# Performance work log

Measured on AMD Instinct MI355X. Metric: run time of the kernel, lower is better.

Reference implementation:

```python
import jax, jax.numpy as jnp
import numpy as np

N, E, D, H, ED = 50000, 600000, 128, 2, 5
C = D // H  # per-head channels = 64


def _lin(k, fan_in, fan_out):
    return jax.random.normal(k, (fan_out, fan_in), jnp.float32) / np.sqrt(fan_in)


def setup_inputs() -> dict:
    key = jax.random.key(0)
    ks = jax.random.split(key, 12)
    return {
        "x": jax.random.normal(ks[0], (N, D), jnp.float32),
        "edge_index": jax.random.randint(ks[1], (2, E), 0, N, dtype=jnp.int32),
        "edge_attr": jax.random.normal(ks[2], (E, ED), jnp.float32),
        "Wq": _lin(ks[3], D, D), "bq": jnp.zeros((D,), jnp.float32),
        "Wk": _lin(ks[4], D, D), "bk": jnp.zeros((D,), jnp.float32),
        "Wv": _lin(ks[5], D, D), "bv": jnp.zeros((D,), jnp.float32),
        "We": _lin(ks[6], ED, D),                       # lin_edge, bias=False in PyG
        "Wskip": _lin(ks[7], D, D), "bskip": jnp.zeros((D,), jnp.float32),
        "Wbeta": _lin(ks[8], 3 * D, 1),                 # lin_beta, bias=False
        "Wproj": _lin(ks[9], D, D), "bproj": jnp.zeros((D,), jnp.float32),
    }


def reference(x, edge_index, edge_attr, Wq, bq, Wk, bk, Wv, bv, We,
              Wskip, bskip, Wbeta, Wproj, bproj):
    src, dst = edge_index[0], edge_index[1]
    # node projections -> [N, H, C]
    q = (x @ Wq.T + bq).reshape(N, H, C)
    k = (x @ Wk.T + bk).reshape(N, H, C)
    v = (x @ Wv.T + bv).reshape(N, H, C)
    e = (edge_attr @ We.T).reshape(E, H, C)
    # gather per-edge, fold in edge features
    kj = k[src] + e                                   # [E, H, C]
    vj = v[src] + e                                   # [E, H, C]
    alpha = (q[dst] * kj).sum(-1) / np.sqrt(C)        # [E, H]
    # segment softmax over edges grouped by dst node
    amax = jax.ops.segment_max(alpha, dst, num_segments=N)   # [N, H]
    ex = jnp.exp(alpha - amax[dst])
    denom = jax.ops.segment_sum(ex, dst, num_segments=N)     # [N, H]
    w = ex / denom[dst]                               # [E, H]
    # scatter-aggregate weighted values, concat heads
    out = jax.ops.segment_sum(vj * w[:, :, None], dst, num_segments=N).reshape(N, D)
    # beta-gated skip connection
    x_r = x @ Wskip.T + bskip
    beta = jax.nn.sigmoid(jnp.concatenate([out, x_r, out - x_r], axis=-1) @ Wbeta.T)  # [N,1]
    out = beta * x_r + (1.0 - beta) * out
    # outer projection (dropout is identity in eval)
    return out @ Wproj.T + bproj
```

## Files before the change

### kernel.cpp

```cpp
#include <hip/hip_runtime.h>
#include <stdint.h>
#include <math.h>

#define D 128
#define EDIM 5
#define QSCALE 0.1803368801111204f

typedef __attribute__((ext_vector_type(8))) short bf16x8;
typedef __attribute__((ext_vector_type(4))) float f32x4;
typedef _Float16 h16x2 __attribute__((ext_vector_type(2)));

__device__ __forceinline__ float fexp2(float x) {
  return __builtin_amdgcn_exp2f(x);
}

__device__ __forceinline__ ushort f2b(float f) {
  union { float f; uint u; } v; v.f = f;
  uint u = v.u;
  return (ushort)((u + 0x7fff + ((u >> 16) & 1)) >> 16);
}
__device__ __forceinline__ float blo(uint u) {
  union { uint u; float f; } v; v.u = u << 16; return v.f;
}
__device__ __forceinline__ float bhi(uint u) {
  union { uint u; float f; } v; v.u = u & 0xffff0000u; return v.f;
}
__device__ __forceinline__ ushort f2h(float f) {
  union { _Float16 h; ushort u; } v; v.h = (_Float16)f;
  return v.u;
}
__device__ __forceinline__ h16x2 u2h(uint u) {
  union { uint u; h16x2 h; } v; v.u = u; return v.h;
}

#if __has_builtin(__builtin_amdgcn_fdot2)
#define FDOT2(a, b, c) __builtin_amdgcn_fdot2((a), (b), (c), false)
#else
#define FDOT2(a, b, c) ((c) + (float)(a)[0] * (float)(b)[0] + (float)(a)[1] * (float)(b)[1])
#endif


__global__ void hist_kernel(const int* __restrict__ ei, int* __restrict__ deg, int E) {
  int e = blockIdx.x * blockDim.x + threadIdx.x;
  if (e < E) atomicAdd(&deg[ei[(size_t)E + e]], 1);
}

__global__ __launch_bounds__(256) void scan_p1(const int* __restrict__ deg,
                                               int* __restrict__ off,
                                               int* __restrict__ blockSum, int n4) {
  __shared__ int waveTot[4];
  int idx = blockIdx.x * 256 + threadIdx.x;
  int4 v = make_int4(0, 0, 0, 0);
  if (idx < n4) v = ((const int4*)deg)[idx];
  int c0 = v.x, c1 = c0 + v.y, c2 = c1 + v.z, c3 = c2 + v.w;
  int tot = c3;
  int lane = threadIdx.x & 63, w = threadIdx.x >> 6;
  int incl = tot;
#pragma unroll
  for (int ofs = 1; ofs < 64; ofs <<= 1) {
    int t = __shfl_up(incl, ofs, 64);
    if (lane >= ofs) incl += t;
  }
  if (lane == 63) waveTot[w] = incl;
  __syncthreads();
  int wbase = 0;
  for (int i = 0; i < w; ++i) wbase += waveTot[i];
  int excl = wbase + incl - tot;
  if (idx < n4) {
    int4 o;
    o.x = excl; o.y = excl + c0; o.z = excl + c1; o.w = excl + c2;
    ((int4*)off)[idx] = o;
  }
  if (threadIdx.x == 255) blockSum[blockIdx.x] = wbase + incl;
}

__global__ void scan_p2(const int* __restrict__ blockSum, int* __restrict__ blockBase,
                        int* __restrict__ off_last, int nb) {
  int lane = threadIdx.x;
  int v = (lane < nb) ? blockSum[lane] : 0;
  int incl = v;
#pragma unroll
  for (int ofs = 1; ofs < 64; ofs <<= 1) {
    int t = __shfl_up(incl, ofs, 64);
    if (lane >= ofs) incl += t;
  }
  if (lane < nb) blockBase[lane] = incl - v;
  if (lane == 63) *off_last = incl;
}

__global__ __launch_bounds__(256) void scan_p3(int* __restrict__ off,
                                               const int* __restrict__ blockBase,
                                               int* __restrict__ cursor, int n4) {
  int idx = blockIdx.x * 256 + threadIdx.x;
  if (idx >= n4) return;
  int b = blockBase[blockIdx.x];
  int4 v = ((int4*)off)[idx];
  v.x += b; v.y += b; v.z += b; v.w += b;
  ((int4*)off)[idx] = v;
  ((int4*)cursor)[idx] = make_int4(0, 0, 0, 0);
}

__global__ void scatter_kernel(const int* __restrict__ ei, const float* __restrict__ ea,
                               const int* __restrict__ off, int* __restrict__ cursor,
                               uint4* __restrict__ easrt, int E) {
  int e = blockIdx.x * blockDim.x + threadIdx.x;
  if (e >= E) return;
  int dst = ei[(size_t)E + e];
  int pos = off[dst] + atomicAdd(&cursor[dst], 1);
  const float* p = ea + (size_t)e * EDIM;
  uint e0 = f2b(p[0]), e1 = f2b(p[1]), e2 = f2b(p[2]), e3 = f2b(p[3]), e4 = f2b(p[4]);
  easrt[pos] = make_uint4(e0 | (e1 << 16), e2 | (e3 << 16), e4, (uint)ei[e]);
}

__global__ void cvt_w_kernel(const float* __restrict__ Wq, const float* __restrict__ Wk,
                             const float* __restrict__ Wv, const float* __restrict__ Wr,
                             const float* __restrict__ bq, const float* __restrict__ bk,
                             const float* __restrict__ bv, const float* __restrict__ br,
                             const float* __restrict__ We, const float* __restrict__ Wp,
                             ushort* __restrict__ Wcat, float* __restrict__ bcat,
                             ushort* __restrict__ Wpb, int* __restrict__ deg, int N) {
  int i = blockIdx.x * blockDim.x + threadIdx.x;
  if (i < N) deg[i] = 0;
  if (i < 512 * D) {
    int r = i >> 7;
    float v;
    if (r < 128)      v = Wq[i] * QSCALE;
    else if (r < 256) v = Wk[i - 128 * D];
    else if (r < 384) v = Wv[i - 256 * D];
    else              v = Wr[i - 384 * D];
    Wcat[i] = f2b(v);
  } else if (i < 512 * D + 128 * D) {
    int ie = i - 512 * D;
    int r = ie >> 7, c = ie & 127;
    int h = r >> 3, j = r & 7;
    float v = 0.f;
    if (h < 2 && j < 5) {
      for (int d = 0; d < 64; ++d) {
        int dd = h * 64 + d;
        v += We[(size_t)dd * EDIM + j] * QSCALE * Wq[(size_t)dd * D + c];
      }
    }
    Wcat[(size_t)(512 + r) * D + c] = f2b(v);
  }
  if (i < D * D) Wpb[i] = f2b(Wp[i]);
  if (i < 512) {
    float v = (i < 128) ? bq[i] * QSCALE
            : (i < 256) ? bk[i - 128]
            : (i < 384) ? bv[i - 256] : br[i - 384];
    bcat[i] = v;
  } else if (i < 640) {
    int t = i - 512;
    int h = t >> 3, j = t & 7;
    float v = 0.f;
    if (h < 2 && j < 5) {
      for (int d = 0; d < 64; ++d) {
        int dd = h * 64 + d;
        v += bq[dd] * QSCALE * We[(size_t)dd * EDIM + j];
      }
    }
    bcat[i] = v;
  }
}

__global__ __launch_bounds__(256) void proj_gemm_kernel(
    const float* __restrict__ x, const ushort* __restrict__ Wcat,
    const float* __restrict__ bcat,
    ushort* __restrict__ q, ushort* __restrict__ kv, ushort* __restrict__ xr,
    float* __restrict__ qwe, int M)
{
  __shared__ __attribute__((aligned(16))) ushort As[64][128];
  __shared__ __attribute__((aligned(16))) ushort Bs[128][128];
  const int tid = threadIdx.x;
  const int rowBase = blockIdx.x * 64;

#pragma unroll
  for (int it = 0; it < 4; ++it) {
    int i = it * 256 + tid;
    int r = i >> 4, c = i & 15;
    int gr = rowBase + r;
    float4 a0 = make_float4(0.f, 0.f, 0.f, 0.f), a1 = a0;
    if (gr < M) {
      a0 = *(const float4*)(x + (size_t)gr * D + c * 8);
      a1 = *(const float4*)(x + (size_t)gr * D + c * 8 + 4);
    }
    uint4 w;
    w.x = (uint)f2b(a0.x) | ((uint)f2b(a0.y) << 16);
    w.y = (uint)f2b(a0.z) | ((uint)f2b(a0.w) << 16);
    w.z = (uint)f2b(a1.x) | ((uint)f2b(a1.y) << 16);
    w.w = (uint)f2b(a1.z) | ((uint)f2b(a1.w) << 16);
    *(uint4*)(&As[r][(c ^ (r & 7)) * 8]) = w;
  }

  const int lane = tid & 63;
  const int wave = tid >> 6;
  const int wm = (wave >> 1) * 32;
  const int wn = (wave & 1) * 64;
  const int lrow = lane & 15;
  const int kgrp = lane >> 4;
  const int orow = (lane >> 4) * 4;
  const int ocol = lane & 15;

  for (int cb = 0; cb < 5; ++cb) {
#pragma unroll
    for (int it = 0; it < 8; ++it) {
      int i = it * 256 + tid;
      int r = i >> 4, c = i & 15;
      if (cb == 4 && r >= 16) continue;
      uint4 bv4 = *(const uint4*)(Wcat + (size_t)(cb * 128 + r) * D + c * 8);
      *(uint4*)(&Bs[r][(c ^ (r & 7)) * 8]) = bv4;
    }
    __syncthreads();

    f32x4 acc[2][4] = {};
#pragma unroll
    for (int ks = 0; ks < 4; ++ks) {
      int chunk = ks * 4 + kgrp;
      bf16x8 a[2], b[4];
#pragma unroll
      for (int m = 0; m < 2; ++m) {
        int r = wm + m * 16 + lrow;
        a[m] = *(const bf16x8*)&As[r][(chunk ^ (r & 7)) * 8];
      }
#pragma unroll
      for (int n = 0; n < 4; ++n) {
        int r = wn + n * 16 + lrow;
        b[n] = *(const bf16x8*)&Bs[r][(chunk ^ (r & 7)) * 8];
      }
#pragma unroll
      for (int m = 0; m < 2; ++m)
#pragma unroll
        for (int n = 0; n < 4; ++n) {
          if (cb == 4 && (wn + n * 16) >= 16) continue;
          acc[m][n] = __builtin_amdgcn_mfma_f32_16x16x32_bf16(a[m], b[n], acc[m][n], 0, 0, 0);
        }
    }

#pragma unroll
    for (int m = 0; m < 2; ++m) {
#pragma unroll
      for (int n = 0; n < 4; ++n) {
        if (cb == 4 && (wn + n * 16) >= 16) continue;
        int col = cb * 128 + wn + n * 16 + ocol;
        float bi = bcat[col];
        int sel = col >> 7, c = col & 127;
#pragma unroll
        for (int ii = 0; ii < 4; ++ii) {
          int gr = rowBase + wm + m * 16 + orow + ii;
          if (gr >= M) continue;
          float v = acc[m][n][ii] + bi;
          if (sel == 0)      q[(size_t)gr * D + c] = f2h(v);
          else if (sel == 1) kv[(size_t)gr * 2 * D + c] = f2h(v);
          else if (sel == 2) kv[(size_t)gr * 2 * D + D + c] = f2h(v);
          else if (sel == 3) xr[(size_t)gr * D + c] = f2b(v);
          else if (c < 16)   qwe[(size_t)gr * 16 + c] = v;
        }
      }
    }
    __syncthreads();
  }
}

__global__ __launch_bounds__(256) void out_gemm_kernel(
    const ushort* __restrict__ g, const ushort* __restrict__ Wpb,
    const float* __restrict__ bp, float* __restrict__ out, int M)
{
  __shared__ __attribute__((aligned(16))) ushort As[64][128];
  __shared__ __attribute__((aligned(16))) ushort Bs[128][128];
  const int tid = threadIdx.x;
  const int rowBase = blockIdx.x * 64;

#pragma unroll
  for (int it = 0; it < 4; ++it) {
    int i = it * 256 + tid;
    int r = i >> 4, c = i & 15;
    int gr = rowBase + r;
    uint4 av = make_uint4(0, 0, 0, 0);
    if (gr < M) av = *(const uint4*)(g + (size_t)gr * D + c * 8);
    *(uint4*)(&As[r][(c ^ (r & 7)) * 8]) = av;
  }
#pragma unroll
  for (int it = 0; it < 8; ++it) {
    int i = it * 256 + tid;
    int r = i >> 4, c = i & 15;
    uint4 bv4 = *(const uint4*)(Wpb + (size_t)r * D + c * 8);
    *(uint4*)(&Bs[r][(c ^ (r & 7)) * 8]) = bv4;
  }
  __syncthreads();

  const int lane = tid & 63;
  const int wave = tid >> 6;
  const int wm = (wave >> 1) * 32;
  const int wn = (wave & 1) * 64;
  const int lrow = lane & 15;
  const int kgrp = lane >> 4;

  f32x4 acc[2][4] = {};
#pragma unroll
  for (int ks = 0; ks < 4; ++ks) {
    int chunk = ks * 4 + kgrp;
    bf16x8 a[2], b[4];
#pragma unroll
    for (int m = 0; m < 2; ++m) {
      int r = wm + m * 16 + lrow;
      a[m] = *(const bf16x8*)&As[r][(chunk ^ (r & 7)) * 8];
    }
#pragma unroll
    for (int n = 0; n < 4; ++n) {
      int r = wn + n * 16 + lrow;
      b[n] = *(const bf16x8*)&Bs[r][(chunk ^ (r & 7)) * 8];
    }
#pragma unroll
    for (int m = 0; m < 2; ++m)
#pragma unroll
      for (int n = 0; n < 4; ++n)
        acc[m][n] = __builtin_amdgcn_mfma_f32_16x16x32_bf16(a[m], b[n], acc[m][n], 0, 0, 0);
  }

  const int orow = (lane >> 4) * 4;
  const int ocol = lane & 15;
#pragma unroll
  for (int m = 0; m < 2; ++m) {
#pragma unroll
    for (int n = 0; n < 4; ++n) {
      int col = wn + n * 16 + ocol;
      float bi = bp[col];
#pragma unroll
      for (int ii = 0; ii < 4; ++ii) {
        int gr = rowBase + wm + m * 16 + orow + ii;
        if (gr >= M) continue;
        out[(size_t)gr * D + col] = acc[m][n][ii] + bi;
      }
    }
  }
}

__global__ __launch_bounds__(256) void node_attn_kernel(
    const ushort* __restrict__ q, const ushort* __restrict__ kv,
    const ushort* __restrict__ xr, ushort* __restrict__ g,
    const float* __restrict__ qwe, const uint4* __restrict__ easrt,
    const float* __restrict__ We, const float* __restrict__ Wb,
    const int* __restrict__ off, int N)
{
  const int wid = threadIdx.x >> 6;
  const int lane = threadIdx.x & 63;
  const int node = blockIdx.x * 4 + wid;
  if (node >= N) return;
  const int grp = lane >> 4;
  const int i = lane & 15;
  const int di = i * 8;
  const int head = i >> 3;

  h16x2 qh[4];
  {
    uint4 qa = *(const uint4*)(q + (size_t)node * D + di);
    qh[0] = u2h(qa.x); qh[1] = u2h(qa.y); qh[2] = u2h(qa.z); qh[3] = u2h(qa.w);
  }
  float qw[5];
  {
    const float* qp = qwe + (size_t)node * 16 + head * 8;
    float4 t = *(const float4*)qp;
    qw[0] = t.x; qw[1] = t.y; qw[2] = t.z; qw[3] = t.w; qw[4] = qp[4];
  }

  const int beg = off[node], end = off[node + 1];
  float m = -INFINITY, s = 0.f;
  float o[8] = {0.f, 0.f, 0.f, 0.f, 0.f, 0.f, 0.f, 0.f};
  float wea[5] = {0.f, 0.f, 0.f, 0.f, 0.f};

  if (beg < end) {
    const int em1 = end - 1;
    const int p0 = beg + grp;
    uint4 e0 = easrt[min(p0, em1)];
    uint4 e1 = easrt[min(p0 + 4, em1)];
    uint4 e2 = easrt[min(p0 + 8, em1)];
    const ushort* kp_;
    kp_ = kv + (size_t)e0.w * (2 * D);
    uint4 k0 = *(const uint4*)(kp_ + di), v0 = *(const uint4*)(kp_ + D + di);
    kp_ = kv + (size_t)e1.w * (2 * D);
    uint4 k1 = *(const uint4*)(kp_ + di), v1 = *(const uint4*)(kp_ + D + di);
    uint4 k2v = k0, v2v = v0;

#define ATT_STEP(PB, eA, eC, kA, vA, kC, vC)                                   \
    {                                                                          \
      int p = (PB) + grp;                                                      \
      bool valid = p < end;                                                    \
      const ushort* kpn = kv + (size_t)(eC).w * (2 * D);                       \
      (kC) = *(const uint4*)(kpn + di);                                        \
      (vC) = *(const uint4*)(kpn + D + di);                                    \
      float ea0 = blo((eA).x), ea1 = bhi((eA).x), ea2 = blo((eA).y),           \
            ea3 = bhi((eA).y), ea4 = blo((eA).z);                              \
      (eA) = easrt[min(p + 12, em1)];                                          \
      float part = FDOT2(qh[0], u2h((kA).x), 0.f);                             \
      part = FDOT2(qh[1], u2h((kA).y), part);                                  \
      part = FDOT2(qh[2], u2h((kA).z), part);                                  \
      part = FDOT2(qh[3], u2h((kA).w), part);                                  \
      part += __shfl_xor(part, 1, 64);                                         \
      part += __shfl_xor(part, 2, 64);                                         \
      part += __shfl_xor(part, 4, 64);                                         \
      float eadot = qw[0] * ea0 + qw[1] * ea1 + qw[2] * ea2 + qw[3] * ea3      \
                  + qw[4] * ea4;                                               \
      float alpha = valid ? (part + eadot) : -INFINITY;                        \
      h16x2 va = u2h((vA).x), vb = u2h((vA).y), vc = u2h((vA).z),              \
            vd = u2h((vA).w);                                                  \
      float vv0 = (float)va[0], vv1 = (float)va[1], vv2 = (float)vb[0],        \
            vv3 = (float)vb[1], vv4 = (float)vc[0], vv5 = (float)vc[1],        \
            vv6 = (float)vd[0], vv7 = (float)vd[1];                            \
      if (__any(alpha > m + 11.5f)) {                                          \
        float nm = fmaxf(m, alpha);                                            \
        float scale = (m > -1e30f) ? fexp2(m - nm) : 0.f;                      \
        float pw = valid ? fexp2(alpha - nm) : 0.f;                            \
        m = nm;                                                                \
        s = s * scale + pw;                                                    \
        o[0] = o[0] * scale + pw * vv0; o[1] = o[1] * scale + pw * vv1;        \
        o[2] = o[2] * scale + pw * vv2; o[3] = o[3] * scale + pw * vv3;        \
        o[4] = o[4] * scale + pw * vv4; o[5] = o[5] * scale + pw * vv5;        \
        o[6] = o[6] * scale + pw * vv6; o[7] = o[7] * scale + pw * vv7;        \
        wea[0] = wea[0] * scale + pw * ea0; wea[1] = wea[1] * scale + pw * ea1;\
        wea[2] = wea[2] * scale + pw * ea2; wea[3] = wea[3] * scale + pw * ea3;\
        wea[4] = wea[4] * scale + pw * ea4;                                    \
      } else {                                                                 \
        float pw = valid ? fexp2(alpha - m) : 0.f;                             \
        s += pw;                                                               \
        o[0] += pw * vv0; o[1] += pw * vv1; o[2] += pw * vv2;                  \
        o[3] += pw * vv3; o[4] += pw * vv4; o[5] += pw * vv5;                  \
        o[6] += pw * vv6; o[7] += pw * vv7;                                    \
        wea[0] += pw * ea0; wea[1] += pw * ea1; wea[2] += pw * ea2;            \
        wea[3] += pw * ea3; wea[4] += pw * ea4;                                \
      }                                                                        \
    }

    for (int pb = beg; pb < end; pb += 12) {
      ATT_STEP(pb,     e0, e2, k0, v0, k2v, v2v)
      ATT_STEP(pb + 4, e1, e0, k1, v1, k0, v0)
      ATT_STEP(pb + 8, e2, e1, k2v, v2v, k1, v1)
    }
#undef ATT_STEP
  }

#pragma unroll
  for (int ofs = 16; ofs < 64; ofs <<= 1) {
    float m2 = __shfl_xor(m, ofs, 64);
    float s2 = __shfl_xor(s, ofs, 64);
    float o2[8], w2[5];
#pragma unroll
    for (int j = 0; j < 8; ++j) o2[j] = __shfl_xor(o[j], ofs, 64);
#pragma unroll
    for (int j = 0; j < 5; ++j) w2[j] = __shfl_xor(wea[j], ofs, 64);
    float nm = fmaxf(m, m2);
    float e1m = (m > -1e30f) ? fexp2(m - nm) : 0.f;
    float e2m = (m2 > -1e30f) ? fexp2(m2 - nm) : 0.f;
    s = s * e1m + s2 * e2m;
#pragma unroll
    for (int j = 0; j < 8; ++j) o[j] = o[j] * e1m + o2[j] * e2m;
#pragma unroll
    for (int j = 0; j < 5; ++j) wea[j] = wea[j] * e1m + w2[j] * e2m;
    m = nm;
  }

  float inv = (s > 0.f) ? (1.f / s) : 0.f;
#pragma unroll
  for (int j = 0; j < 8; ++j) o[j] *= inv;
#pragma unroll
  for (int j = 0; j < 5; ++j) wea[j] *= inv;

  {
    const float* wp = We + (size_t)di * EDIM;
    float4 w[10];
#pragma unroll
    for (int t = 0; t < 10; ++t) w[t] = *(const float4*)(wp + 4 * t);
#pragma unroll
    for (int r = 0; r < 8; ++r)
#pragma unroll
      for (int j = 0; j < 5; ++j) {
        int idx = r * 5 + j;
        o[r] += wea[j] * ((const float*)&w[idx >> 2])[idx & 3];
      }
  }

  float xrv[8];
  {
    uint4 xa = *(const uint4*)(xr + (size_t)node * D + di);
    xrv[0] = blo(xa.x); xrv[1] = bhi(xa.x); xrv[2] = blo(xa.y); xrv[3] = bhi(xa.y);
    xrv[4] = blo(xa.z); xrv[5] = bhi(xa.z); xrv[6] = blo(xa.w); xrv[7] = bhi(xa.w);
  }
  float part = 0.f;
#pragma unroll
  for (int r = 0; r < 8; ++r) {
    float w1 = Wb[di + r] + Wb[256 + di + r];
    float w2 = Wb[128 + di + r] - Wb[256 + di + r];
    part += o[r] * w1 + xrv[r] * w2;
  }
#pragma unroll
  for (int ofs = 1; ofs < 16; ofs <<= 1) part += __shfl_xor(part, ofs, 64);
  float beta = 1.f / (1.f + __expf(-part));

  if (grp == 0) {
    uint pk[4];
#pragma unroll
    for (int r = 0; r < 4; ++r) {
      float g0 = beta * xrv[2 * r] + (1.f - beta) * o[2 * r];
      float g1 = beta * xrv[2 * r + 1] + (1.f - beta) * o[2 * r + 1];
      pk[r] = (uint)f2b(g0) | ((uint)f2b(g1) << 16);
    }
    *(uint4*)(g + (size_t)node * D + di) = make_uint4(pk[0], pk[1], pk[2], pk[3]);
  }
}


extern "C" void kernel_launch(void* const* d_in, const int* in_sizes, int n_in,
                              void* d_out, int out_size, void* d_ws, size_t ws_size,
                              hipStream_t stream)
{
  const float* x  = (const float*)d_in[0];
  const int*   ei = (const int*)d_in[1];
  const float* ea = (const float*)d_in[2];
  const float* Wq = (const float*)d_in[3];
  const float* bq = (const float*)d_in[4];
  const float* Wk = (const float*)d_in[5];
  const float* bk = (const float*)d_in[6];
  const float* Wv = (const float*)d_in[7];
  const float* bv = (const float*)d_in[8];
  const float* We = (const float*)d_in[9];
  const float* Wr = (const float*)d_in[10];
  const float* br = (const float*)d_in[11];
  const float* Wb = (const float*)d_in[12];
  const float* Wp = (const float*)d_in[13];
  const float* bp = (const float*)d_in[14];

  const int N = in_sizes[0] / D;
  const int E = in_sizes[1] / 2;
  float* out = (float*)d_out;

  char* ws = (char*)d_ws;
  size_t o = 0;
  auto alloc = [&](size_t bytes) -> void* {
    void* p = ws + o;
    o = (o + bytes + 255) & ~(size_t)255;
    return p;
  };
  ushort* q      = (ushort*)alloc((size_t)N * D * sizeof(ushort));
  ushort* kv     = (ushort*)alloc((size_t)N * 2 * D * sizeof(ushort));
  ushort* xr     = (ushort*)alloc((size_t)N * D * sizeof(ushort));
  ushort* g      = (ushort*)alloc((size_t)N * D * sizeof(ushort));
  float*  qwe    = (float*)alloc((size_t)N * 16 * sizeof(float));
  ushort* Wcat   = (ushort*)alloc((size_t)640 * D * sizeof(ushort));
  float*  bcat   = (float*)alloc(640 * sizeof(float));
  ushort* Wpb    = (ushort*)alloc((size_t)D * D * sizeof(ushort));
  int*    deg    = (int*)alloc((size_t)N * sizeof(int));
  int*    cursor = (int*)alloc((size_t)N * sizeof(int));
  int*    offs   = (int*)alloc((size_t)(N + 1) * sizeof(int));
  uint4*  easrt  = (uint4*)alloc((size_t)E * sizeof(uint4));
  int*    bsum   = (int*)alloc(64 * sizeof(int));
  int*    bbase  = (int*)alloc(64 * sizeof(int));

  const int n4 = N / 4;
  const int nb = (n4 + 255) / 256;

  cvt_w_kernel<<<(512 * D + 128 * D + 255) / 256, 256, 0, stream>>>(
      Wq, Wk, Wv, Wr, bq, bk, bv, br, We, Wp, Wcat, bcat, Wpb, deg, N);

  hist_kernel<<<(E + 255) / 256, 256, 0, stream>>>(ei, deg, E);
  scan_p1<<<nb, 256, 0, stream>>>(deg, offs, bsum, n4);
  scan_p2<<<1, 64, 0, stream>>>(bsum, bbase, offs + N, nb);
  scan_p3<<<nb, 256, 0, stream>>>(offs, bbase, cursor, n4);
  scatter_kernel<<<(E + 255) / 256, 256, 0, stream>>>(ei, ea, offs, cursor, easrt, E);

  proj_gemm_kernel<<<(N + 63) / 64, 256, 0, stream>>>(x, Wcat, bcat, q, kv, xr, qwe, N);

  node_attn_kernel<<<(N + 3) / 4, 256, 0, stream>>>(q, kv, xr, g, qwe, easrt, We, Wb,
                                                    offs, N);

  out_gemm_kernel<<<(N + 63) / 64, 256, 0, stream>>>(g, Wpb, bp, out, N);
}
```

Before: 214.4 us.

## Quantize q and kv to int8 with per-node scales for attention gather

Adds a quantization kernel that converts the fp16 q and k/v node projections to int8 using one scale per node (q scale as float, kv scale as fp16). The per-source kv scale is packed into the sorted edge records by the scatter kernel, which now runs after projection. The attention kernel computes q·k with sdot4 integer dot products and dequantizes v in registers. This halves the bytes fetched per gathered edge, at the cost of an extra pass over q/kv and reduced numerical accuracy from coarse per-node int8 scaling.

```diff
diff --git a/kernel.cpp b/kernel.cpp
--- a/kernel.cpp
+++ b/kernel.cpp
@@ -29,14 +29,24 @@
   union { _Float16 h; ushort u; } v; v.h = (_Float16)f;
   return v.u;
 }
+__device__ __forceinline__ float h2f(ushort u) {
+  union { ushort u; _Float16 h; } v; v.u = u; return (float)v.h;
+}
 __device__ __forceinline__ h16x2 u2h(uint u) {
   union { uint u; h16x2 h; } v; v.u = u; return v.h;
 }
 
-#if __has_builtin(__builtin_amdgcn_fdot2)
-#define FDOT2(a, b, c) __builtin_amdgcn_fdot2((a), (b), (c), false)
+#if __has_builtin(__builtin_amdgcn_sdot4)
+#define SDOT4(a, b, c) __builtin_amdgcn_sdot4((int)(a), (int)(b), (c), false)
 #else
-#define FDOT2(a, b, c) ((c) + (float)(a)[0] * (float)(b)[0] + (float)(a)[1] * (float)(b)[1])
+__device__ __forceinline__ int sdot4_fb(uint a, uint b, int c) {
+  c += ((int)(a << 24) >> 24) * ((int)(b << 24) >> 24);
+  c += ((int)(a << 16) >> 24) * ((int)(b << 16) >> 24);
+  c += ((int)(a << 8) >> 24) * ((int)(b << 8) >> 24);
+  c += ((int)a >> 24) * ((int)b >> 24);
+  return c;
+}
+#define SDOT4(a, b, c) sdot4_fb((a), (b), (c))
 #endif
 
 
@@ -102,14 +112,17 @@
 
 __global__ void scatter_kernel(const int* __restrict__ ei, const float* __restrict__ ea,
                                const int* __restrict__ off, int* __restrict__ cursor,
+                               const ushort* __restrict__ kvscale,
                                uint4* __restrict__ easrt, int E) {
   int e = blockIdx.x * blockDim.x + threadIdx.x;
   if (e >= E) return;
   int dst = ei[(size_t)E + e];
+  int src = ei[e];
   int pos = off[dst] + atomicAdd(&cursor[dst], 1);
   const float* p = ea + (size_t)e * EDIM;
   uint e0 = f2b(p[0]), e1 = f2b(p[1]), e2 = f2b(p[2]), e3 = f2b(p[3]), e4 = f2b(p[4]);
-  easrt[pos] = make_uint4(e0 | (e1 << 16), e2 | (e3 << 16), e4, (uint)ei[e]);
+  uint sv = kvscale[src];
+  easrt[pos] = make_uint4(e0 | (e1 << 16), e2 | (e3 << 16), e4 | (sv << 16), (uint)src);
 }
 
 __global__ void cvt_w_kernel(const float* __restrict__ Wq, const float* __restrict__ Wk,
@@ -260,6 +273,50 @@
   }
 }
 
+__global__ __launch_bounds__(256) void quant_kernel(
+    const ushort* __restrict__ q, const ushort* __restrict__ kv,
+    uchar* __restrict__ q8, uchar* __restrict__ kv8,
+    float* __restrict__ qscale, ushort* __restrict__ kvscale, int N)
+{
+  const int wid = threadIdx.x >> 6;
+  const int lane = threadIdx.x & 63;
+  const int node = blockIdx.x * 4 + wid;
+  if (node >= N) return;
+
+  uint qu = *(const uint*)(q + (size_t)node * D + lane * 2);
+  h16x2 qh = u2h(qu);
+  float q0 = (float)qh[0], q1 = (float)qh[1];
+  float qm = fmaxf(fabsf(q0), fabsf(q1));
+
+  uint2 kvu = *(const uint2*)(kv + (size_t)node * 2 * D + lane * 4);
+  h16x2 a = u2h(kvu.x), b = u2h(kvu.y);
+  float f0 = (float)a[0], f1 = (float)a[1], f2 = (float)b[0], f3 = (float)b[1];
+  float km = fmaxf(fmaxf(fabsf(f0), fabsf(f1)), fmaxf(fabsf(f2), fabsf(f3)));
+
+#pragma unroll
+  for (int ofs = 1; ofs < 64; ofs <<= 1) {
+    qm = fmaxf(qm, __shfl_xor(qm, ofs, 64));
+    km = fmaxf(km, __shfl_xor(km, ofs, 64));
+  }
+  float qinv = (qm > 0.f) ? 127.f / qm : 0.f;
+  float kinv = (km > 0.f) ? 127.f / km : 0.f;
+
+  int t0 = (int)__builtin_rintf(q0 * qinv), t1 = (int)__builtin_rintf(q1 * qinv);
+  *(ushort*)(q8 + (size_t)node * D + lane * 2) =
+      (ushort)((t0 & 255) | ((t1 & 255) << 8));
+
+  int s0 = (int)__builtin_rintf(f0 * kinv), s1 = (int)__builtin_rintf(f1 * kinv);
+  int s2 = (int)__builtin_rintf(f2 * kinv), s3 = (int)__builtin_rintf(f3 * kinv);
+  *(uint*)(kv8 + (size_t)node * 2 * D + lane * 4) =
+      (uint)(s0 & 255) | ((uint)(s1 & 255) << 8) | ((uint)(s2 & 255) << 16) |
+      ((uint)(s3 & 255) << 24);
+
+  if (lane == 0) {
+    qscale[node] = qm * (1.f / 127.f);
+    kvscale[node] = f2h(km * (1.f / 127.f));
+  }
+}
+
 __global__ __launch_bounds__(256) void out_gemm_kernel(
     const ushort* __restrict__ g, const ushort* __restrict__ Wpb,
     const float* __restrict__ bp, float* __restrict__ out, int M)
@@ -335,7 +392,8 @@
 }
 
 __global__ __launch_bounds__(256) void node_attn_kernel(
-    const ushort* __restrict__ q, const ushort* __restrict__ kv,
+    const uchar* __restrict__ q8, const uchar* __restrict__ kv8,
+    const float* __restrict__ qscale,
     const ushort* __restrict__ xr, ushort* __restrict__ g,
     const float* __restrict__ qwe, const uint4* __restrict__ easrt,
     const float* __restrict__ We, const float* __restrict__ Wb,
@@ -350,11 +408,8 @@
   const int di = i * 8;
   const int head = i >> 3;
 
-  h16x2 qh[4];
-  {
-    uint4 qa = *(const uint4*)(q + (size_t)node * D + di);
-    qh[0] = u2h(qa.x); qh[1] = u2h(qa.y); qh[2] = u2h(qa.z); qh[3] = u2h(qa.w);
-  }
+  uint2 q8u = *(const uint2*)(q8 + (size_t)node * D + di);
+  const float qs = qscale[node];
   float qw[5];
   {
     const float* qp = qwe + (size_t)node * 16 + head * 8;
@@ -373,57 +428,61 @@
     uint4 e0 = easrt[min(p0, em1)];
     uint4 e1 = easrt[min(p0 + 4, em1)];
     uint4 e2 = easrt[min(p0 + 8, em1)];
-    const ushort* kp_;
-    kp_ = kv + (size_t)e0.w * (2 * D);
-    uint4 k0 = *(const uint4*)(kp_ + di), v0 = *(const uint4*)(kp_ + D + di);
-    kp_ = kv + (size_t)e1.w * (2 * D);
-    uint4 k1 = *(const uint4*)(kp_ + di), v1 = *(const uint4*)(kp_ + D + di);
-    uint4 k2v = k0, v2v = v0;
+    const uchar* kp_;
+    kp_ = kv8 + (size_t)e0.w * 256;
+    uint2 k0 = *(const uint2*)(kp_ + di), v0 = *(const uint2*)(kp_ + 128 + di);
+    kp_ = kv8 + (size_t)e1.w * 256;
+    uint2 k1 = *(const uint2*)(kp_ + di), v1 = *(const uint2*)(kp_ + 128 + di);
+    uint2 k2v = k0, v2v = v0;
 
 #define ATT_STEP(PB, eA, eC, kA, vA, kC, vC)                                   \
     {                                                                          \
       int p = (PB) + grp;                                                      \
       bool valid = p < end;                                                    \
-      const ushort* kpn = kv + (size_t)(eC).w * (2 * D);                       \
-      (kC) = *(const uint4*)(kpn + di);                                        \
-      (vC) = *(const uint4*)(kpn + D + di);                                    \
+      const uchar* kpn = kv8 + (size_t)(eC).w * 256;                           \
+      (kC) = *(const uint2*)(kpn + di);                                        \
+      (vC) = *(const uint2*)(kpn + 128 + di);                                  \
       float ea0 = blo((eA).x), ea1 = bhi((eA).x), ea2 = blo((eA).y),           \
             ea3 = bhi((eA).y), ea4 = blo((eA).z);                              \
+      float ss = h2f((ushort)((eA).z >> 16));                                  \
       (eA) = easrt[min(p + 12, em1)];                                          \
-      float part = FDOT2(qh[0], u2h((kA).x), 0.f);                             \
-      part = FDOT2(qh[1], u2h((kA).y), part);                                  \
-      part = FDOT2(qh[2], u2h((kA).z), part);                                  \
-      part = FDOT2(qh[3], u2h((kA).w), part);                                  \
-      part += __shfl_xor(part, 1, 64);                                         \
-      part += __shfl_xor(part, 2, 64);                                         \
-      part += __shfl_xor(part, 4, 64);                                         \
+      int idot = SDOT4((kA).x, q8u.x, 0);                                      \
+      idot = SDOT4((kA).y, q8u.y, idot);                                       \
+      idot += __shfl_xor(idot, 1, 64);                                         \
+      idot += __shfl_xor(idot, 2, 64);                                         \
+      idot += __shfl_xor(idot, 4, 64);                                         \
       float eadot = qw[0] * ea0 + qw[1] * ea1 + qw[2] * ea2 + qw[3] * ea3      \
                   + qw[4] * ea4;                                               \
-      float alpha = valid ? (part + eadot) : -INFINITY;                        \
-      h16x2 va = u2h((vA).x), vb = u2h((vA).y), vc = u2h((vA).z),              \
-            vd = u2h((vA).w);                                                  \
-      float vv0 = (float)va[0], vv1 = (float)va[1], vv2 = (float)vb[0],        \
-            vv3 = (float)vb[1], vv4 = (float)vc[0], vv5 = (float)vc[1],        \
-            vv6 = (float)vd[0], vv7 = (float)vd[1];                            \
+      float alpha = valid ? (qs * ss * (float)idot + eadot) : -INFINITY;       \
+      float vv0 = (float)((int)((vA).x << 24) >> 24);                          \
+      float vv1 = (float)((int)((vA).x << 16) >> 24);                          \
+      float vv2 = (float)((int)((vA).x << 8) >> 24);                           \
+      float vv3 = (float)((int)(vA).x >> 24);                                  \
+      float vv4 = (float)((int)((vA).y << 24) >> 24);                          \
+      float vv5 = (float)((int)((vA).y << 16) >> 24);                          \
+      float vv6 = (float)((int)((vA).y << 8) >> 24);                           \
+      float vv7 = (float)((int)(vA).y >> 24);                                  \
       if (__any(alpha > m + 11.5f)) {                                          \
         float nm = fmaxf(m, alpha);                                            \
         float scale = (m > -1e30f) ? fexp2(m - nm) : 0.f;                      \
         float pw = valid ? fexp2(alpha - nm) : 0.f;                            \
+        float pws = pw * ss;                                                   \
         m = nm;                                                                \
         s = s * scale + pw;                                                    \
-        o[0] = o[0] * scale + pw * vv0; o[1] = o[1] * scale + pw * vv1;        \
-        o[2] = o[2] * scale + pw * vv2; o[3] = o[3] * scale + pw * vv3;        \
-        o[4] = o[4] * scale + pw * vv4; o[5] = o[5] * scale + pw * vv5;        \
-        o[6] = o[6] * scale + pw * vv6; o[7] = o[7] * scale + pw * vv7;        \
+        o[0] = o[0] * scale + pws * vv0; o[1] = o[1] * scale + pws * vv1;      \
+        o[2] = o[2] * scale + pws * vv2; o[3] = o[3] * scale + pws * vv3;      \
+        o[4] = o[4] * scale + pws * vv4; o[5] = o[5] * scale + pws * vv5;      \
+        o[6] = o[6] * scale + pws * vv6; o[7] = o[7] * scale + pws * vv7;      \
         wea[0] = wea[0] * scale + pw * ea0; wea[1] = wea[1] * scale + pw * ea1;\
         wea[2] = wea[2] * scale + pw * ea2; wea[3] = wea[3] * scale + pw * ea3;\
         wea[4] = wea[4] * scale + pw * ea4;                                    \
       } else {                                                                 \
         float pw = valid ? fexp2(alpha - m) : 0.f;                             \
+        float pws = pw * ss;                                                   \
         s += pw;                                                               \
-        o[0] += pw * vv0; o[1] += pw * vv1; o[2] += pw * vv2;                  \
-        o[3] += pw * vv3; o[4] += pw * vv4; o[5] += pw * vv5;                  \
-        o[6] += pw * vv6; o[7] += pw * vv7;                                    \
+        o[0] += pws * vv0; o[1] += pws * vv1; o[2] += pws * vv2;               \
+        o[3] += pws * vv3; o[4] += pws * vv4; o[5] += pws * vv5;               \
+        o[6] += pws * vv6; o[7] += pws * vv7;                                  \
         wea[0] += pw * ea0; wea[1] += pw * ea1; wea[2] += pw * ea2;            \
         wea[3] += pw * ea3; wea[4] += pw * ea4;                                \
       }                                                                        \
@@ -538,20 +597,24 @@
     o = (o + bytes + 255) & ~(size_t)255;
     return p;
   };
-  ushort* q      = (ushort*)alloc((size_t)N * D * sizeof(ushort));
-  ushort* kv     = (ushort*)alloc((size_t)N * 2 * D * sizeof(ushort));
-  ushort* xr     = (ushort*)alloc((size_t)N * D * sizeof(ushort));
-  ushort* g      = (ushort*)alloc((size_t)N * D * sizeof(ushort));
-  float*  qwe    = (float*)alloc((size_t)N * 16 * sizeof(float));
-  ushort* Wcat   = (ushort*)alloc((size_t)640 * D * sizeof(ushort));
-  float*  bcat   = (float*)alloc(640 * sizeof(float));
-  ushort* Wpb    = (ushort*)alloc((size_t)D * D * sizeof(ushort));
-  int*    deg    = (int*)alloc((size_t)N * sizeof(int));
-  int*    cursor = (int*)alloc((size_t)N * sizeof(int));
-  int*    offs   = (int*)alloc((size_t)(N + 1) * sizeof(int));
-  uint4*  easrt  = (uint4*)alloc((size_t)E * sizeof(uint4));
-  int*    bsum   = (int*)alloc(64 * sizeof(int));
-  int*    bbase  = (int*)alloc(64 * sizeof(int));
+  ushort* q       = (ushort*)alloc((size_t)N * D * sizeof(ushort));
+  ushort* kv      = (ushort*)alloc((size_t)N * 2 * D * sizeof(ushort));
+  uchar*  q8      = (uchar*)alloc((size_t)N * D);
+  uchar*  kv8     = (uchar*)alloc((size_t)N * 2 * D);
+  float*  qscale  = (float*)alloc((size_t)N * sizeof(float));
+  ushort* kvscale = (ushort*)alloc((size_t)N * sizeof(ushort));
+  ushort* xr      = (ushort*)alloc((size_t)N * D * sizeof(ushort));
+  ushort* g       = (ushort*)alloc((size_t)N * D * sizeof(ushort));
+  float*  qwe     = (float*)alloc((size_t)N * 16 * sizeof(float));
+  ushort* Wcat    = (ushort*)alloc((size_t)640 * D * sizeof(ushort));
+  float*  bcat    = (float*)alloc(640 * sizeof(float));
+  ushort* Wpb     = (ushort*)alloc((size_t)D * D * sizeof(ushort));
+  int*    deg     = (int*)alloc((size_t)N * sizeof(int));
+  int*    cursor  = (int*)alloc((size_t)N * sizeof(int));
+  int*    offs    = (int*)alloc((size_t)(N + 1) * sizeof(int));
+  uint4*  easrt   = (uint4*)alloc((size_t)E * sizeof(uint4));
+  int*    bsum    = (int*)alloc(64 * sizeof(int));
+  int*    bbase   = (int*)alloc(64 * sizeof(int));
 
   const int n4 = N / 4;
   const int nb = (n4 + 255) / 256;
@@ -563,12 +626,16 @@
   scan_p1<<<nb, 256, 0, stream>>>(deg, offs, bsum, n4);
   scan_p2<<<1, 64, 0, stream>>>(bsum, bbase, offs + N, nb);
   scan_p3<<<nb, 256, 0, stream>>>(offs, bbase, cursor, n4);
-  scatter_kernel<<<(E + 255) / 256, 256, 0, stream>>>(ei, ea, offs, cursor, easrt, E);
 
   proj_gemm_kernel<<<(N + 63) / 64, 256, 0, stream>>>(x, Wcat, bcat, q, kv, xr, qwe, N);
 
-  node_attn_kernel<<<(N + 3) / 4, 256, 0, stream>>>(q, kv, xr, g, qwe, easrt, We, Wb,
-                                                    offs, N);
+  quant_kernel<<<(N + 3) / 4, 256, 0, stream>>>(q, kv, q8, kv8, qscale, kvscale, N);
+
+  scatter_kernel<<<(E + 255) / 256, 256, 0, stream>>>(ei, ea, offs, cursor, kvscale,
+                                                      easrt, E);
+
+  node_attn_kernel<<<(N + 3) / 4, 256, 0, stream>>>(q8, kv8, qscale, xr, g, qwe, easrt,
+                                                    We, Wb, offs, N);
 
   out_gemm_kernel<<<(N + 63) / 64, 256, 0, stream>>>(g, Wpb, bp, out, N);
 }
```

Result: slower. 223.5 us (+4.2%).

## Sort nodes by in-degree so attention waves in a block have balanced work

Applied to the files above, without the earlier changes.

Builds a degree histogram and counting-sort permutation of nodes. The attention kernel processes nodes in degree-sorted order, so waves in the same block get similar edge counts. To keep the attention kernel's q, xr and qwe reads contiguous, the projection GEMM writes them in permuted order, and the output GEMM scatters rows back through the permutation. This adds three small kernels, two histogram atomics passes and scattered row stores in both GEMMs in exchange for less load imbalance and tail divergence.

```diff
diff --git a/kernel.cpp b/kernel.cpp
--- a/kernel.cpp
+++ b/kernel.cpp
@@ -90,7 +90,9 @@
 
 __global__ __launch_bounds__(256) void scan_p3(int* __restrict__ off,
                                                const int* __restrict__ blockBase,
-                                               int* __restrict__ cursor, int n4) {
+                                               int* __restrict__ cursor,
+                                               const int* __restrict__ deg,
+                                               int* __restrict__ dhist, int n4) {
   int idx = blockIdx.x * 256 + threadIdx.x;
   if (idx >= n4) return;
   int b = blockBase[blockIdx.x];
@@ -98,6 +100,29 @@
   v.x += b; v.y += b; v.z += b; v.w += b;
   ((int4*)off)[idx] = v;
   ((int4*)cursor)[idx] = make_int4(0, 0, 0, 0);
+  int4 dv = ((const int4*)deg)[idx];
+  atomicAdd(&dhist[min(dv.x, 128)], 1);
+  atomicAdd(&dhist[min(dv.y, 128)], 1);
+  atomicAdd(&dhist[min(dv.z, 128)], 1);
+  atomicAdd(&dhist[min(dv.w, 128)], 1);
+}
+
+__global__ void dscan_kernel(const int* __restrict__ dhist, int* __restrict__ dbase) {
+  if (threadIdx.x == 0) {
+    int acc = 0;
+    for (int i = 0; i < 129; ++i) { dbase[i] = acc; acc += dhist[i]; }
+  }
+}
+
+__global__ void dscatter_kernel(const int* __restrict__ deg, const int* __restrict__ dbase,
+                                int* __restrict__ dcur, int* __restrict__ perm,
+                                int* __restrict__ inv, int N) {
+  int n = blockIdx.x * blockDim.x + threadIdx.x;
+  if (n >= N) return;
+  int b = min(deg[n], 128);
+  int pos = dbase[b] + atomicAdd(&dcur[b], 1);
+  perm[pos] = n;
+  inv[n] = pos;
 }
 
 __global__ void scatter_kernel(const int* __restrict__ ei, const float* __restrict__ ea,
@@ -118,9 +143,11 @@
                              const float* __restrict__ bv, const float* __restrict__ br,
                              const float* __restrict__ We, const float* __restrict__ Wp,
                              ushort* __restrict__ Wcat, float* __restrict__ bcat,
-                             ushort* __restrict__ Wpb, int* __restrict__ deg, int N) {
+                             ushort* __restrict__ Wpb, int* __restrict__ deg,
+                             int* __restrict__ dhist, int* __restrict__ dcur, int N) {
   int i = blockIdx.x * blockDim.x + threadIdx.x;
   if (i < N) deg[i] = 0;
+  if (i < 129) { dhist[i] = 0; dcur[i] = 0; }
   if (i < 512 * D) {
     int r = i >> 7;
     float v;
@@ -164,7 +191,7 @@
 
 __global__ __launch_bounds__(256) void proj_gemm_kernel(
     const float* __restrict__ x, const ushort* __restrict__ Wcat,
-    const float* __restrict__ bcat,
+    const float* __restrict__ bcat, const int* __restrict__ inv,
     ushort* __restrict__ q, ushort* __restrict__ kv, ushort* __restrict__ xr,
     float* __restrict__ qwe, int M)
 {
@@ -248,11 +275,11 @@
           int gr = rowBase + wm + m * 16 + orow + ii;
           if (gr >= M) continue;
           float v = acc[m][n][ii] + bi;
-          if (sel == 0)      q[(size_t)gr * D + c] = f2h(v);
+          if (sel == 0)      q[(size_t)inv[gr] * D + c] = f2h(v);
           else if (sel == 1) kv[(size_t)gr * 2 * D + c] = f2h(v);
           else if (sel == 2) kv[(size_t)gr * 2 * D + D + c] = f2h(v);
-          else if (sel == 3) xr[(size_t)gr * D + c] = f2b(v);
-          else if (c < 16)   qwe[(size_t)gr * 16 + c] = v;
+          else if (sel == 3) xr[(size_t)inv[gr] * D + c] = f2b(v);
+          else if (c < 16)   qwe[(size_t)inv[gr] * 16 + c] = v;
         }
       }
     }
@@ -262,7 +289,8 @@
 
 __global__ __launch_bounds__(256) void out_gemm_kernel(
     const ushort* __restrict__ g, const ushort* __restrict__ Wpb,
-    const float* __restrict__ bp, float* __restrict__ out, int M)
+    const float* __restrict__ bp, const int* __restrict__ perm,
+    float* __restrict__ out, int M)
 {
   __shared__ __attribute__((aligned(16))) ushort As[64][128];
   __shared__ __attribute__((aligned(16))) ushort Bs[128][128];
@@ -328,7 +356,7 @@
       for (int ii = 0; ii < 4; ++ii) {
         int gr = rowBase + wm + m * 16 + orow + ii;
         if (gr >= M) continue;
-        out[(size_t)gr * D + col] = acc[m][n][ii] + bi;
+        out[(size_t)perm[gr] * D + col] = acc[m][n][ii] + bi;
       }
     }
   }
@@ -339,12 +367,13 @@
     const ushort* __restrict__ xr, ushort* __restrict__ g,
     const float* __restrict__ qwe, const uint4* __restrict__ easrt,
     const float* __restrict__ We, const float* __restrict__ Wb,
-    const int* __restrict__ off, int N)
+    const int* __restrict__ off, const int* __restrict__ perm, int N)
 {
   const int wid = threadIdx.x >> 6;
   const int lane = threadIdx.x & 63;
-  const int node = blockIdx.x * 4 + wid;
-  if (node >= N) return;
+  const int slot = blockIdx.x * 4 + wid;
+  if (slot >= N) return;
+  const int node = perm[slot];
   const int grp = lane >> 4;
   const int i = lane & 15;
   const int di = i * 8;
@@ -352,12 +381,12 @@
 
   h16x2 qh[4];
   {
-    uint4 qa = *(const uint4*)(q + (size_t)node * D + di);
+    uint4 qa = *(const uint4*)(q + (size_t)slot * D + di);
     qh[0] = u2h(qa.x); qh[1] = u2h(qa.y); qh[2] = u2h(qa.z); qh[3] = u2h(qa.w);
   }
   float qw[5];
   {
-    const float* qp = qwe + (size_t)node * 16 + head * 8;
+    const float* qp = qwe + (size_t)slot * 16 + head * 8;
     float4 t = *(const float4*)qp;
     qw[0] = t.x; qw[1] = t.y; qw[2] = t.z; qw[3] = t.w; qw[4] = qp[4];
   }
@@ -457,11 +486,11 @@
     m = nm;
   }
 
-  float inv = (s > 0.f) ? (1.f / s) : 0.f;
-#pragma unroll
-  for (int j = 0; j < 8; ++j) o[j] *= inv;
-#pragma unroll
-  for (int j = 0; j < 5; ++j) wea[j] *= inv;
+  float inv_s = (s > 0.f) ? (1.f / s) : 0.f;
+#pragma unroll
+  for (int j = 0; j < 8; ++j) o[j] *= inv_s;
+#pragma unroll
+  for (int j = 0; j < 5; ++j) wea[j] *= inv_s;
 
   {
     const float* wp = We + (size_t)di * EDIM;
@@ -479,7 +508,7 @@
 
   float xrv[8];
   {
-    uint4 xa = *(const uint4*)(xr + (size_t)node * D + di);
+    uint4 xa = *(const uint4*)(xr + (size_t)slot * D + di);
     xrv[0] = blo(xa.x); xrv[1] = bhi(xa.x); xrv[2] = blo(xa.y); xrv[3] = bhi(xa.y);
     xrv[4] = blo(xa.z); xrv[5] = bhi(xa.z); xrv[6] = blo(xa.w); xrv[7] = bhi(xa.w);
   }
@@ -502,7 +531,7 @@
       float g1 = beta * xrv[2 * r + 1] + (1.f - beta) * o[2 * r + 1];
       pk[r] = (uint)f2b(g0) | ((uint)f2b(g1) << 16);
     }
-    *(uint4*)(g + (size_t)node * D + di) = make_uint4(pk[0], pk[1], pk[2], pk[3]);
+    *(uint4*)(g + (size_t)slot * D + di) = make_uint4(pk[0], pk[1], pk[2], pk[3]);
   }
 }
 
@@ -552,23 +581,32 @@
   uint4*  easrt  = (uint4*)alloc((size_t)E * sizeof(uint4));
   int*    bsum   = (int*)alloc(64 * sizeof(int));
   int*    bbase  = (int*)alloc(64 * sizeof(int));
+  int*    dhist  = (int*)alloc(129 * sizeof(int));
+  int*    dbase  = (int*)alloc(129 * sizeof(int));
+  int*    dcur   = (int*)alloc(129 * sizeof(int));
+  int*    perm   = (int*)alloc((size_t)N * sizeof(int));
+  int*    invp   = (int*)alloc((size_t)N * sizeof(int));
 
   const int n4 = N / 4;
   const int nb = (n4 + 255) / 256;
 
   cvt_w_kernel<<<(512 * D + 128 * D + 255) / 256, 256, 0, stream>>>(
-      Wq, Wk, Wv, Wr, bq, bk, bv, br, We, Wp, Wcat, bcat, Wpb, deg, N);
+      Wq, Wk, Wv, Wr, bq, bk, bv, br, We, Wp, Wcat, bcat, Wpb, deg, dhist, dcur, N);
 
   hist_kernel<<<(E + 255) / 256, 256, 0, stream>>>(ei, deg, E);
   scan_p1<<<nb, 256, 0, stream>>>(deg, offs, bsum, n4);
   scan_p2<<<1, 64, 0, stream>>>(bsum, bbase, offs + N, nb);
-  scan_p3<<<nb, 256, 0, stream>>>(offs, bbase, cursor, n4);
+  scan_p3<<<nb, 256, 0, stream>>>(offs, bbase, cursor, deg, dhist, n4);
+  dscan_kernel<<<1, 64, 0, stream>>>(dhist, dbase);
+  dscatter_kernel<<<(N + 255) / 256, 256, 0, stream>>>(deg, dbase, dcur, perm, invp, N);
+
+  proj_gemm_kernel<<<(N + 63) / 64, 256, 0, stream>>>(x, Wcat, bcat, invp,
+                                                      q, kv, xr, qwe, N);
+
   scatter_kernel<<<(E + 255) / 256, 256, 0, stream>>>(ei, ea, offs, cursor, easrt, E);
 
-  proj_gemm_kernel<<<(N + 63) / 64, 256, 0, stream>>>(x, Wcat, bcat, q, kv, xr, qwe, N);
-
   node_attn_kernel<<<(N + 3) / 4, 256, 0, stream>>>(q, kv, xr, g, qwe, easrt, We, Wb,
-                                                    offs, N);
-
-  out_gemm_kernel<<<(N + 63) / 64, 256, 0, stream>>>(g, Wpb, bp, out, N);
-}
+                                                    offs, perm, N);
+
+  out_gemm_kernel<<<(N + 63) / 64, 256, 0, stream>>>(g, Wpb, bp, perm, out, N);
+}
```

Measured after the change: 542.9 us. +153.2%, slower.
